# Optimization experiments

Measured on AMD Instinct MI355X. Metric: run time of the kernel, lower is better.

## Reference

```python
import jax, jax.numpy as jnp
import numpy as np

L, N, H_IN, H = 512, 32, 1024, 1024


def _mk_params(key, in_dim, hid):
    ks = jax.random.split(key, 7)
    s_in = 1.0 / np.sqrt(in_dim)
    s_h = 1.0 / np.sqrt(hid)
    return dict(
        Wmx=jax.random.uniform(ks[0], (hid, in_dim), jnp.float32, -s_in, s_in),
        Wmh=jax.random.uniform(ks[1], (hid, hid), jnp.float32, -s_h, s_h),
        bmx=jax.random.uniform(ks[2], (hid,), jnp.float32, -s_in, s_in),
        bmh=jax.random.uniform(ks[3], (hid,), jnp.float32, -s_h, s_h),
        Wgx=jax.random.uniform(ks[4], (4 * hid, in_dim), jnp.float32, -s_in, s_in),
        Wgm=jax.random.uniform(ks[5], (4 * hid, hid), jnp.float32, -s_h, s_h),
        bg=jax.random.uniform(ks[6], (4 * hid,), jnp.float32, -s_h, s_h),
    )


def setup_inputs() -> dict:
    key = jax.random.key(0)
    k_in, k0, k1 = jax.random.split(key, 3)
    inp = {"inputs": jax.random.normal(k_in, (L, N, H_IN), jnp.float32)}
    for i, (k, d) in enumerate([(k0, H_IN), (k1, H)]):
        p = _mk_params(k, d, H)
        for name, v in p.items():
            inp[f"{name}{i}"] = v
    return inp


def _run_layer(xs, state, Wmx, Wmh, bmx, bmh, Wgx, Wgm, bg):
    # xs: (L, N, in_dim); state: ((N,H),(N,H))
    def step(carry, x_t):
        h, c = carry
        m = (x_t @ Wmx.T + bmx) * (h @ Wmh.T + bmh)  # multiplicative intermediate
        g = x_t @ Wgx.T + m @ Wgm.T + bg             # (N, 4H)
        i_g, f_g, z_g, o_g = jnp.split(g, 4, axis=-1)
        c_new = jax.nn.sigmoid(f_g) * c + jax.nn.sigmoid(i_g) * jnp.tanh(z_g)
        h_new = jax.nn.sigmoid(o_g) * jnp.tanh(c_new)
        return (h_new, c_new), h_new

    (h, c), ys = jax.lax.scan(step, state, xs)
    return ys, (h, c)


def reference(inputs, Wmx0, Wmh0, bmx0, bmh0, Wgx0, Wgm0, bg0,
              Wmx1, Wmh1, bmx1, bmh1, Wgx1, Wgm1, bg1):
    zeros = jnp.zeros((N, H), inputs.dtype)
    state = (zeros, zeros)
    # NOTE: original torch code carries hidden_state across layers (quirk kept).
    ys, state = _run_layer(inputs, state, Wmx0, Wmh0, bmx0, bmh0, Wgx0, Wgm0, bg0)
    hs, cs = [state[0]], [state[1]]
    ys, state = _run_layer(ys, state, Wmx1, Wmh1, bmx1, bmh1, Wgx1, Wgm1, bg1)
    hs.append(state[0]); cs.append(state[1])
    return ys, (jnp.stack(hs), jnp.stack(cs))
```

## Files before the change

### kernel.cpp

```cpp
#include <hip/hip_runtime.h>
#include <hip/hip_bf16.h>


typedef unsigned short u16;
typedef unsigned int u32;
typedef unsigned long long u64;
typedef __attribute__((ext_vector_type(8))) short bf16x8;
typedef __attribute__((ext_vector_type(4))) float f32x4;

#define LSEQ 512
#define NB   32
#define HD   1024
#define G4   4096
#define YSZ  (LSEQ*NB*HD)
#define NH32 (NB*HD)
#define SEG  64
#define NSEG (LSEQ/SEG)
#define PERSIST_LDS 163840

#define ATOMIC_RLX __ATOMIC_RELAXED
#define SCOPE_AGT __HIP_MEMORY_SCOPE_AGENT

__device__ __forceinline__ float b2f(u16 u) {
    u32 i = ((u32)u) << 16; float f; __builtin_memcpy(&f, &i, 4); return f;
}
__device__ __forceinline__ u16 f2b(float f) {
    u32 x; __builtin_memcpy(&x, &f, 4);
    return (u16)((x + 0x7fffu + ((x >> 16) & 1u)) >> 16);
}
__device__ __forceinline__ int SW(int row, int byte) { return byte ^ ((row & 7) << 4); }

__device__ __forceinline__ void waitpair(const u32* flags, u32 target) {
    const int lane = threadIdx.x & 63;
    const u64* p = (const u64*)flags + (size_t)lane * 16;
    for (;;) {
        u64 v = __hip_atomic_load(p, ATOMIC_RLX, SCOPE_AGT);
        u32 lo = (u32)v, hi = (u32)(v >> 32);
        if (__all(lo >= target && hi >= target)) break;
    }
    asm volatile("" ::: "memory");
}
__device__ __forceinline__ void signal_slot(u32* flags, int b, int rt, u32 val) {
    asm volatile("s_waitcnt vmcnt(0)" ::: "memory");
    if ((threadIdx.x & 63) == 0)
        __hip_atomic_store(flags + b * 32 + rt, val, ATOMIC_RLX, SCOPE_AGT);
}

__global__ void k_cvt(const float* __restrict__ s, u16* __restrict__ d, long n) {
    long i = (long)blockIdx.x * blockDim.x + threadIdx.x;
    long stride = (long)gridDim.x * blockDim.x;
    for (; i < n; i += stride) d[i] = f2b(s[i]);
}

template<typename XT> __device__ __forceinline__ bf16x8 ld8(const XT* p);
template<> __device__ __forceinline__ bf16x8 ld8<u16>(const u16* p) {
    return *(const bf16x8*)p;
}
template<> __device__ __forceinline__ bf16x8 ld8<float>(const float* p) {
    float4 a = *(const float4*)p, b = *(const float4*)(p + 4);
    bf16x8 r;
    r[0]=(short)f2b(a.x); r[1]=(short)f2b(a.y); r[2]=(short)f2b(a.z); r[3]=(short)f2b(a.w);
    r[4]=(short)f2b(b.x); r[5]=(short)f2b(b.y); r[6]=(short)f2b(b.z); r[7]=(short)f2b(b.w);
    return r;
}

template<typename XT>
__global__ __launch_bounds__(256) void k_gemm(
    const XT* __restrict__ X, const u16* __restrict__ W,
    const float* __restrict__ bias, u16* __restrict__ Out, int ldo)
{
    __shared__ u16 As[128][40];
    __shared__ u16 Bs[128][40];
    int bm = blockIdx.y, bn = blockIdx.x;
    int tid = threadIdx.x;
    int w = tid >> 6, lane = tid & 63;
    int wm = w >> 1, wn = w & 1;
    int l16 = lane & 15, lk = lane >> 4;

    f32x4 acc[4][4];
    #pragma unroll
    for (int i = 0; i < 4; ++i)
        #pragma unroll
        for (int j = 0; j < 4; ++j) acc[i][j] = (f32x4){0.f, 0.f, 0.f, 0.f};

    for (int kt = 0; kt < 32; ++kt) {
        __syncthreads();
        #pragma unroll
        for (int c = 0; c < 2; ++c) {
            int cid = tid + c * 256;
            int rrow = cid >> 2, kc = (cid & 3) * 8;
            *(bf16x8*)(&As[rrow][kc]) = ld8<XT>(X + (long)(bm * 128 + rrow) * HD + kt * 32 + kc);
            *(bf16x8*)(&Bs[rrow][kc]) = ld8<u16>(W + (long)(bn * 128 + rrow) * HD + kt * 32 + kc);
        }
        __syncthreads();
        bf16x8 af[4], bfr[4];
        #pragma unroll
        for (int mt = 0; mt < 4; ++mt)
            af[mt] = *(const bf16x8*)(&As[wm * 64 + mt * 16 + l16][lk * 8]);
        #pragma unroll
        for (int nt = 0; nt < 4; ++nt)
            bfr[nt] = *(const bf16x8*)(&Bs[wn * 64 + nt * 16 + l16][lk * 8]);
        #pragma unroll
        for (int mt = 0; mt < 4; ++mt)
            #pragma unroll
            for (int nt = 0; nt < 4; ++nt)
                acc[mt][nt] = __builtin_amdgcn_mfma_f32_16x16x32_bf16(
                    af[mt], bfr[nt], acc[mt][nt], 0, 0, 0);
    }
    #pragma unroll
    for (int mt = 0; mt < 4; ++mt)
        #pragma unroll
        for (int nt = 0; nt < 4; ++nt) {
            int colg = bn * 128 + wn * 64 + nt * 16 + l16;
            float bv = bias[colg];
            #pragma unroll
            for (int r = 0; r < 4; ++r) {
                int rowg = bm * 128 + wm * 64 + mt * 16 + lk * 4 + r;
                Out[(long)rowg * ldo + colg] = f2b(acc[mt][nt][r] + bv);
            }
        }
}

__global__ __launch_bounds__(256, 1) void k_persist(
    const u16* __restrict__ Wmhb, const float* __restrict__ bmh,
    const u16* __restrict__ Wgmb,
    const u16* __restrict__ Ab,
    const u16* __restrict__ Gxb,
    u16* eh, u16* em,
    float* __restrict__ cbuf,
    u16* __restrict__ yb, float* __restrict__ yf,
    float* __restrict__ tail,
    int l, int tbc, int tbi, u32* fM, u32* fH)
{
    extern __shared__ __align__(16) char lds[];
    const int tid = threadIdx.x;
    const int b = blockIdx.x;
    const int w = tid >> 6, lane = tid & 63;
    const int l16 = lane & 15, lk = lane >> 4;

    for (int it = 0; it < 32; ++it) {
        int cch = tid + it * 256;
        int lr = cch >> 7, k8 = cch & 127;
        int g = lr >> 4, c16 = lr & 15;
        bf16x8 v = *(const bf16x8*)(Wgmb + (long)(g * 1024 + 16 * b + c16) * HD + k8 * 8);
        *(bf16x8*)(lds + SW(lr, lr * 2048 + k8 * 16)) = v;
    }
    for (int it = 0; it < 8; ++it) {
        int cch = tid + it * 256;
        int lr = cch >> 7, k8 = cch & 127;
        bf16x8 v = *(const bf16x8*)(Wmhb + (long)(16 * b + lr) * HD + k8 * 8);
        *(bf16x8*)(lds + 131072 + SW(lr, lr * 2048 + k8 * 16)) = v;
    }
    __syncthreads();

    const int colg = 16 * b + l16;

    if (w >= 2) {
        const int rt = w - 2;
        const float bcol = bmh[colg];
        const u64* hrow = (const u64*)eh + (rt * 16 + l16) * (HD / 4);
        u16* mdst = em + (rt * 16 + lk * 4) * HD + colg;

        for (int t = 0; t < SEG; ++t) {
            const u32 gt = (u32)(tbc + t);
            const u16* At = Ab + (long)(tbi + t) * NH32;
            u16 atv[4];
            #pragma unroll
            for (int r = 0; r < 4; ++r)
                atv[r] = At[(rt * 16 + lk * 4 + r) * HD + colg];
            waitpair(fH, gt);
            u64 hq[64];
            #pragma unroll
            for (int kt = 0; kt < 32; ++kt) {
                hq[2*kt]   = __hip_atomic_load(hrow + kt * 8 + lk * 2,     ATOMIC_RLX, SCOPE_AGT);
                hq[2*kt+1] = __hip_atomic_load(hrow + kt * 8 + lk * 2 + 1, ATOMIC_RLX, SCOPE_AGT);
            }
            __builtin_amdgcn_sched_barrier(0);
            f32x4 acc = (f32x4){0.f, 0.f, 0.f, 0.f};
            #pragma unroll
            for (int kt = 0; kt < 32; ++kt) {
                union { bf16x8 v; u64 q[2]; } u;
                u.q[0] = hq[2*kt]; u.q[1] = hq[2*kt+1];
                bf16x8 bfrag = *(const bf16x8*)(lds + 131072 +
                                SW(l16, l16 * 2048 + kt * 64 + lk * 16));
                acc = __builtin_amdgcn_mfma_f32_16x16x32_bf16(u.v, bfrag, acc, 0, 0, 0);
            }
            #pragma unroll
            for (int r = 0; r < 4; ++r)
                __hip_atomic_store(mdst + r * HD,
                    f2b(b2f(atv[r]) * (acc[r] + bcol)), ATOMIC_RLX, SCOPE_AGT);
            signal_slot(fM, b, rt, gt + 1);
        }
    } else {
        const int rt = w;
        f32x4 creg;
        #pragma unroll
        for (int r = 0; r < 4; ++r)
            creg[r] = cbuf[(rt * 16 + lk * 4 + r) * HD + colg];
        const u64* mrow = (const u64*)em + (rt * 16 + l16) * (HD / 4);

        for (int t = 0; t < SEG; ++t) {
            const u32 gt = (u32)(tbc + t);
            const u16* Gx = Gxb + (long)t * NB * G4;
            u16 gxv[4][4];
            #pragma unroll
            for (int g = 0; g < 4; ++g)
                #pragma unroll
                for (int r = 0; r < 4; ++r)
                    gxv[g][r] = Gx[(long)(rt * 16 + lk * 4 + r) * G4 + g * 1024 + colg];
            waitpair(fM, gt + 1);
            u64 mq[64];
            #pragma unroll
            for (int kt = 0; kt < 32; ++kt) {
                mq[2*kt]   = __hip_atomic_load(mrow + kt * 8 + lk * 2,     ATOMIC_RLX, SCOPE_AGT);
                mq[2*kt+1] = __hip_atomic_load(mrow + kt * 8 + lk * 2 + 1, ATOMIC_RLX, SCOPE_AGT);
            }
            __builtin_amdgcn_sched_barrier(0);
            f32x4 acc[4];
            #pragma unroll
            for (int g = 0; g < 4; ++g) acc[g] = (f32x4){0.f, 0.f, 0.f, 0.f};
            #pragma unroll
            for (int kt = 0; kt < 32; ++kt) {
                union { bf16x8 v; u64 q[2]; } u;
                u.q[0] = mq[2*kt]; u.q[1] = mq[2*kt+1];
                #pragma unroll
                for (int g = 0; g < 4; ++g) {
                    int lr = g * 16 + l16;
                    bf16x8 bfrag = *(const bf16x8*)(lds + SW(lr, lr * 2048 + kt * 64 + lk * 16));
                    acc[g] = __builtin_amdgcn_mfma_f32_16x16x32_bf16(u.v, bfrag, acc[g], 0, 0, 0);
                }
            }
            float hn[4];
            #pragma unroll
            for (int r = 0; r < 4; ++r) {
                int row = rt * 16 + lk * 4 + r;
                float ig = acc[0][r] + b2f(gxv[0][r]);
                float fg = acc[1][r] + b2f(gxv[1][r]);
                float zg = acc[2][r] + b2f(gxv[2][r]);
                float og = acc[3][r] + b2f(gxv[3][r]);
                float si = 1.f / (1.f + expf(-ig));
                float sf = 1.f / (1.f + expf(-fg));
                float so = 1.f / (1.f + expf(-og));
                float cn = sf * creg[r] + si * tanhf(zg);
                hn[r] = so * tanhf(cn);
                creg[r] = cn;
                __hip_atomic_store(eh + (long)row * HD + colg, f2b(hn[r]), ATOMIC_RLX, SCOPE_AGT);
            }
            signal_slot(fH, b, rt, gt + 1);
            #pragma unroll
            for (int r = 0; r < 4; ++r) {
                int row = rt * 16 + lk * 4 + r;
                long yidx = (long)(tbi + t) * NH32 + (long)row * HD + colg;
                if (yb) yb[yidx] = f2b(hn[r]); else yf[yidx] = hn[r];
                if (tbi + t == LSEQ - 1) {
                    tail[(long)l * NH32 + row * HD + colg] = hn[r];
                    tail[2L * NH32 + (long)l * NH32 + row * HD + colg] = creg[r];
                }
            }
        }
        #pragma unroll
        for (int r = 0; r < 4; ++r)
            cbuf[(rt * 16 + lk * 4 + r) * HD + colg] = creg[r];
    }
}

extern "C" void kernel_launch(void* const* d_in, const int* in_sizes, int n_in,
                              void* d_out, int out_size, void* d_ws, size_t ws_size,
                              hipStream_t stream) {
    (void)in_sizes; (void)n_in; (void)out_size; (void)ws_size;
    const float* inputs = (const float*)d_in[0];
    const float* Wmx[2] = {(const float*)d_in[1], (const float*)d_in[8]};
    const float* Wmh[2] = {(const float*)d_in[2], (const float*)d_in[9]};
    const float* bmx[2] = {(const float*)d_in[3], (const float*)d_in[10]};
    const float* bmh[2] = {(const float*)d_in[4], (const float*)d_in[11]};
    const float* Wgx[2] = {(const float*)d_in[5], (const float*)d_in[12]};
    const float* Wgm[2] = {(const float*)d_in[6], (const float*)d_in[13]};
    const float* bg[2]  = {(const float*)d_in[7], (const float*)d_in[14]};
    float* out = (float*)d_out;

    char* ws = (char*)d_ws;
    const long MB = 1024L * 1024L;
    u16* Wmxb[2] = {(u16*)(ws + 0 * MB),  (u16*)(ws + 2 * MB)};
    u16* Wmhb[2] = {(u16*)(ws + 4 * MB),  (u16*)(ws + 6 * MB)};
    u16* Wgxb[2] = {(u16*)(ws + 8 * MB),  (u16*)(ws + 16 * MB)};
    u16* Wgmb[2] = {(u16*)(ws + 24 * MB), (u16*)(ws + 32 * MB)};
    u16* Yb  = (u16*)(ws + 40 * MB);
    u16* Ab  = (u16*)(ws + 72 * MB);
    u16* Gxb = (u16*)(ws + 104 * MB);
    char* ex = ws + 120 * MB;
    u16* exch_h = (u16*)ex;
    u16* exch_m = (u16*)(ex + 65536);
    float* cbuf = (float*)(ex + 131072);
    u32* fM     = (u32*)(ex + 262144);
    u32* fH     = (u32*)(ex + 262144 + 8192);

    hipFuncSetAttribute((const void*)k_persist,
                        hipFuncAttributeMaxDynamicSharedMemorySize, PERSIST_LDS);

    hipMemsetAsync(ex, 0, 262144 + 16384, stream);

    k_cvt<<<512, 256, 0, stream>>>(Wmx[0], Wmxb[0], (long)HD * HD);
    k_cvt<<<512, 256, 0, stream>>>(Wmx[1], Wmxb[1], (long)HD * HD);
    k_cvt<<<512, 256, 0, stream>>>(Wmh[0], Wmhb[0], (long)HD * HD);
    k_cvt<<<512, 256, 0, stream>>>(Wmh[1], Wmhb[1], (long)HD * HD);
    k_cvt<<<1024, 256, 0, stream>>>(Wgx[0], Wgxb[0], (long)G4 * HD);
    k_cvt<<<1024, 256, 0, stream>>>(Wgx[1], Wgxb[1], (long)G4 * HD);
    k_cvt<<<1024, 256, 0, stream>>>(Wgm[0], Wgmb[0], (long)G4 * HD);
    k_cvt<<<1024, 256, 0, stream>>>(Wgm[1], Wgmb[1], (long)G4 * HD);

    for (int l = 0; l < 2; ++l) {
        if (l == 0)
            k_gemm<float><<<dim3(8, 128), 256, 0, stream>>>(inputs, Wmxb[0], bmx[0], Ab, HD);
        else
            k_gemm<u16><<<dim3(8, 128), 256, 0, stream>>>(Yb, Wmxb[1], bmx[1], Ab, HD);
        for (int s = 0; s < NSEG; ++s) {
            if (l == 0)
                k_gemm<float><<<dim3(32, 16), 256, 0, stream>>>(
                    inputs + (long)s * SEG * NB * HD, Wgxb[0], bg[0], Gxb, G4);
            else
                k_gemm<u16><<<dim3(32, 16), 256, 0, stream>>>(
                    Yb + (long)s * SEG * NB * HD, Wgxb[1], bg[1], Gxb, G4);
            k_persist<<<64, 256, PERSIST_LDS, stream>>>(
                Wmhb[l], bmh[l], Wgmb[l], Ab, Gxb,
                exch_h, exch_m, cbuf,
                l ? nullptr : Yb, l ? out : nullptr, out + YSZ,
                l, l * LSEQ + s * SEG, s * SEG, fM, fH);
        }
    }
}
```

Measured before the change: 15.43 ms.

## Split batch into 8-row sub-blocks so each wave runs both m and gate stages

Instead of dedicating two waves to the m = Ax*(Wmh h) stage and two to the gate stage, each wave now handles both stages on different 8-row sub-blocks (sbA for m, sbB for gates), with per-sub-block flags. This aims to pipeline the two dependent stages across sub-blocks so waves no longer sit idle waiting on the other role. It uses 16-row MFMAs with only half the lanes active on output, which wastes MFMA throughput and adds per-step flag polling.

```diff
diff --git a/kernel.cpp b/kernel.cpp
--- a/kernel.cpp
+++ b/kernel.cpp
@@ -30,20 +30,18 @@
 }
 __device__ __forceinline__ int SW(int row, int byte) { return byte ^ ((row & 7) << 4); }
 
-__device__ __forceinline__ void waitpair(const u32* flags, u32 target) {
-    const int lane = threadIdx.x & 63;
-    const u64* p = (const u64*)flags + (size_t)lane * 16;
+__device__ __forceinline__ void poll_sb(const u32* flags, int sb, u32 target) {
+    const u32* p = flags + (threadIdx.x & 63) * 32 + sb;
     for (;;) {
-        u64 v = __hip_atomic_load(p, ATOMIC_RLX, SCOPE_AGT);
-        u32 lo = (u32)v, hi = (u32)(v >> 32);
-        if (__all(lo >= target && hi >= target)) break;
+        u32 v = __hip_atomic_load(p, ATOMIC_RLX, SCOPE_AGT);
+        if (__all(v >= target)) break;
     }
     asm volatile("" ::: "memory");
 }
-__device__ __forceinline__ void signal_slot(u32* flags, int b, int rt, u32 val) {
+__device__ __forceinline__ void sig_sb(u32* flags, int b, int sb, u32 val) {
     asm volatile("s_waitcnt vmcnt(0)" ::: "memory");
     if ((threadIdx.x & 63) == 0)
-        __hip_atomic_store(flags + b * 32 + rt, val, ATOMIC_RLX, SCOPE_AGT);
+        __hip_atomic_store(flags + b * 32 + sb, val, ATOMIC_RLX, SCOPE_AGT);
 }
 
 __global__ void k_cvt(const float* __restrict__ s, u16* __restrict__ d, long n) {
@@ -154,90 +152,91 @@
     __syncthreads();
 
     const int colg = 16 * b + l16;
-
-    if (w >= 2) {
-        const int rt = w - 2;
-        const float bcol = bmh[colg];
-        const u64* hrow = (const u64*)eh + (rt * 16 + l16) * (HD / 4);
-        u16* mdst = em + (rt * 16 + lk * 4) * HD + colg;
-
-        for (int t = 0; t < SEG; ++t) {
-            const u32 gt = (u32)(tbc + t);
-            const u16* At = Ab + (long)(tbi + t) * NH32;
-            u16 atv[4];
+    const int sbA = w;
+    const int sbB = (w + 2) & 3;
+    const float bcol = bmh[colg];
+    const bool act = (lk < 2);
+    const int lr8 = lk * 4;
+
+    f32x4 creg = (f32x4){0.f, 0.f, 0.f, 0.f};
+    if (act)
+        #pragma unroll
+        for (int r = 0; r < 4; ++r)
+            creg[r] = cbuf[(sbB * 8 + lr8 + r) * HD + colg];
+
+    const u64* hrowA = (const u64*)eh + (sbA * 8 + (l16 & 7)) * (HD / 4);
+    const u64* mrowB = (const u64*)em + (sbB * 8 + (l16 & 7)) * (HD / 4);
+
+    for (int t = 0; t < SEG; ++t) {
+        const u32 gt = (u32)(tbc + t);
+        const u16* At = Ab + (long)(tbi + t) * NH32;
+        const u16* Gx = Gxb + (long)t * NB * G4;
+        u16 atv[4];
+        u16 gxv[4][4];
+        #pragma unroll
+        for (int r = 0; r < 4; ++r)
+            atv[r] = At[(sbA * 8 + ((lr8 + r) & 7)) * HD + colg];
+        #pragma unroll
+        for (int g = 0; g < 4; ++g)
             #pragma unroll
             for (int r = 0; r < 4; ++r)
-                atv[r] = At[(rt * 16 + lk * 4 + r) * HD + colg];
-            waitpair(fH, gt);
-            u64 hq[64];
-            #pragma unroll
-            for (int kt = 0; kt < 32; ++kt) {
-                hq[2*kt]   = __hip_atomic_load(hrow + kt * 8 + lk * 2,     ATOMIC_RLX, SCOPE_AGT);
-                hq[2*kt+1] = __hip_atomic_load(hrow + kt * 8 + lk * 2 + 1, ATOMIC_RLX, SCOPE_AGT);
+                gxv[g][r] = Gx[(long)(sbB * 8 + ((lr8 + r) & 7)) * G4 + g * 1024 + colg];
+
+        poll_sb(fH, sbA, gt);
+        u64 hq[64];
+        #pragma unroll
+        for (int kt = 0; kt < 32; ++kt) {
+            hq[2*kt]   = __hip_atomic_load(hrowA + kt * 8 + lk * 2,     ATOMIC_RLX, SCOPE_AGT);
+            hq[2*kt+1] = __hip_atomic_load(hrowA + kt * 8 + lk * 2 + 1, ATOMIC_RLX, SCOPE_AGT);
+        }
+        __builtin_amdgcn_sched_barrier(0);
+        f32x4 acc = (f32x4){0.f, 0.f, 0.f, 0.f};
+        #pragma unroll
+        for (int kt = 0; kt < 32; ++kt) {
+            union { bf16x8 v; u64 q[2]; } u;
+            u.q[0] = hq[2*kt]; u.q[1] = hq[2*kt+1];
+            bf16x8 bfrag = *(const bf16x8*)(lds + 131072 +
+                            SW(l16, l16 * 2048 + kt * 64 + lk * 16));
+            acc = __builtin_amdgcn_mfma_f32_16x16x32_bf16(u.v, bfrag, acc, 0, 0, 0);
+        }
+        if (act)
+            #pragma unroll
+            for (int r = 0; r < 4; ++r)
+                __hip_atomic_store(em + (long)(sbA * 8 + lr8 + r) * HD + colg,
+                    f2b(b2f(atv[r]) * (acc[r] + bcol)), ATOMIC_RLX, SCOPE_AGT);
+        sig_sb(fM, b, sbA, gt + 1);
+
+        poll_sb(fM, sbB, gt + 1);
+        u64 mq[64];
+        #pragma unroll
+        for (int kt = 0; kt < 32; ++kt) {
+            mq[2*kt]   = __hip_atomic_load(mrowB + kt * 8 + lk * 2,     ATOMIC_RLX, SCOPE_AGT);
+            mq[2*kt+1] = __hip_atomic_load(mrowB + kt * 8 + lk * 2 + 1, ATOMIC_RLX, SCOPE_AGT);
+        }
+        __builtin_amdgcn_sched_barrier(0);
+        f32x4 gacc[4];
+        #pragma unroll
+        for (int g = 0; g < 4; ++g) gacc[g] = (f32x4){0.f, 0.f, 0.f, 0.f};
+        #pragma unroll
+        for (int kt = 0; kt < 32; ++kt) {
+            union { bf16x8 v; u64 q[2]; } u;
+            u.q[0] = mq[2*kt]; u.q[1] = mq[2*kt+1];
+            #pragma unroll
+            for (int g = 0; g < 4; ++g) {
+                int lr = g * 16 + l16;
+                bf16x8 bfrag = *(const bf16x8*)(lds + SW(lr, lr * 2048 + kt * 64 + lk * 16));
+                gacc[g] = __builtin_amdgcn_mfma_f32_16x16x32_bf16(u.v, bfrag, gacc[g], 0, 0, 0);
             }
-            __builtin_amdgcn_sched_barrier(0);
-            f32x4 acc = (f32x4){0.f, 0.f, 0.f, 0.f};
-            #pragma unroll
-            for (int kt = 0; kt < 32; ++kt) {
-                union { bf16x8 v; u64 q[2]; } u;
-                u.q[0] = hq[2*kt]; u.q[1] = hq[2*kt+1];
-                bf16x8 bfrag = *(const bf16x8*)(lds + 131072 +
-                                SW(l16, l16 * 2048 + kt * 64 + lk * 16));
-                acc = __builtin_amdgcn_mfma_f32_16x16x32_bf16(u.v, bfrag, acc, 0, 0, 0);
-            }
-            #pragma unroll
-            for (int r = 0; r < 4; ++r)
-                __hip_atomic_store(mdst + r * HD,
-                    f2b(b2f(atv[r]) * (acc[r] + bcol)), ATOMIC_RLX, SCOPE_AGT);
-            signal_slot(fM, b, rt, gt + 1);
-        }
-    } else {
-        const int rt = w;
-        f32x4 creg;
-        #pragma unroll
-        for (int r = 0; r < 4; ++r)
-            creg[r] = cbuf[(rt * 16 + lk * 4 + r) * HD + colg];
-        const u64* mrow = (const u64*)em + (rt * 16 + l16) * (HD / 4);
-
-        for (int t = 0; t < SEG; ++t) {
-            const u32 gt = (u32)(tbc + t);
-            const u16* Gx = Gxb + (long)t * NB * G4;
-            u16 gxv[4][4];
-            #pragma unroll
-            for (int g = 0; g < 4; ++g)
-                #pragma unroll
-                for (int r = 0; r < 4; ++r)
-                    gxv[g][r] = Gx[(long)(rt * 16 + lk * 4 + r) * G4 + g * 1024 + colg];
-            waitpair(fM, gt + 1);
-            u64 mq[64];
-            #pragma unroll
-            for (int kt = 0; kt < 32; ++kt) {
-                mq[2*kt]   = __hip_atomic_load(mrow + kt * 8 + lk * 2,     ATOMIC_RLX, SCOPE_AGT);
-                mq[2*kt+1] = __hip_atomic_load(mrow + kt * 8 + lk * 2 + 1, ATOMIC_RLX, SCOPE_AGT);
-            }
-            __builtin_amdgcn_sched_barrier(0);
-            f32x4 acc[4];
-            #pragma unroll
-            for (int g = 0; g < 4; ++g) acc[g] = (f32x4){0.f, 0.f, 0.f, 0.f};
-            #pragma unroll
-            for (int kt = 0; kt < 32; ++kt) {
-                union { bf16x8 v; u64 q[2]; } u;
-                u.q[0] = mq[2*kt]; u.q[1] = mq[2*kt+1];
-                #pragma unroll
-                for (int g = 0; g < 4; ++g) {
-                    int lr = g * 16 + l16;
-                    bf16x8 bfrag = *(const bf16x8*)(lds + SW(lr, lr * 2048 + kt * 64 + lk * 16));
-                    acc[g] = __builtin_amdgcn_mfma_f32_16x16x32_bf16(u.v, bfrag, acc[g], 0, 0, 0);
-                }
-            }
-            float hn[4];
+        }
+        float hn[4];
+        if (act) {
             #pragma unroll
             for (int r = 0; r < 4; ++r) {
-                int row = rt * 16 + lk * 4 + r;
-                float ig = acc[0][r] + b2f(gxv[0][r]);
-                float fg = acc[1][r] + b2f(gxv[1][r]);
-                float zg = acc[2][r] + b2f(gxv[2][r]);
-                float og = acc[3][r] + b2f(gxv[3][r]);
+                int row = sbB * 8 + lr8 + r;
+                float ig = gacc[0][r] + b2f(gxv[0][r]);
+                float fg = gacc[1][r] + b2f(gxv[1][r]);
+                float zg = gacc[2][r] + b2f(gxv[2][r]);
+                float og = gacc[3][r] + b2f(gxv[3][r]);
                 float si = 1.f / (1.f + expf(-ig));
                 float sf = 1.f / (1.f + expf(-fg));
                 float so = 1.f / (1.f + expf(-og));
@@ -246,10 +245,12 @@
                 creg[r] = cn;
                 __hip_atomic_store(eh + (long)row * HD + colg, f2b(hn[r]), ATOMIC_RLX, SCOPE_AGT);
             }
-            signal_slot(fH, b, rt, gt + 1);
+        }
+        sig_sb(fH, b, sbB, gt + 1);
+        if (act) {
             #pragma unroll
             for (int r = 0; r < 4; ++r) {
-                int row = rt * 16 + lk * 4 + r;
+                int row = sbB * 8 + lr8 + r;
                 long yidx = (long)(tbi + t) * NH32 + (long)row * HD + colg;
                 if (yb) yb[yidx] = f2b(hn[r]); else yf[yidx] = hn[r];
                 if (tbi + t == LSEQ - 1) {
@@ -258,10 +259,11 @@
                 }
             }
         }
+    }
+    if (act)
         #pragma unroll
         for (int r = 0; r < 4; ++r)
-            cbuf[(rt * 16 + lk * 4 + r) * HD + colg] = creg[r];
-    }
+            cbuf[(sbB * 8 + lr8 + r) * HD + colg] = creg[r];
 }
 
 extern "C" void kernel_launch(void* const* d_in, const int* in_sizes, int n_in,
```

Result: slower. 20.22 ms (+31.1%).

## Poll flags with one wave per block and broadcast via block barriers

Applied to the files above, without the earlier changes.

Before, every wave polled the global flag array itself. Now only one wave per block polls (with s_sleep backoff) and then releases the other waves through __syncthreads. The two role-specialised loops are merged into one loop, so all waves go through the same barriers each step. This cuts global polling traffic, but it adds two block-wide barriers per timestep and removes overlap between the m-producing and gate-computing waves inside a block.

```diff
diff --git a/kernel.cpp b/kernel.cpp
--- a/kernel.cpp
+++ b/kernel.cpp
@@ -30,20 +30,16 @@
 }
 __device__ __forceinline__ int SW(int row, int byte) { return byte ^ ((row & 7) << 4); }
 
-__device__ __forceinline__ void waitpair(const u32* flags, u32 target) {
+__device__ __forceinline__ void pollwait(const u32* flags, u32 target) {
     const int lane = threadIdx.x & 63;
     const u64* p = (const u64*)flags + (size_t)lane * 16;
     for (;;) {
         u64 v = __hip_atomic_load(p, ATOMIC_RLX, SCOPE_AGT);
         u32 lo = (u32)v, hi = (u32)(v >> 32);
         if (__all(lo >= target && hi >= target)) break;
+        __builtin_amdgcn_s_sleep(4);
     }
     asm volatile("" ::: "memory");
-}
-__device__ __forceinline__ void signal_slot(u32* flags, int b, int rt, u32 val) {
-    asm volatile("s_waitcnt vmcnt(0)" ::: "memory");
-    if ((threadIdx.x & 63) == 0)
-        __hip_atomic_store(flags + b * 32 + rt, val, ATOMIC_RLX, SCOPE_AGT);
 }
 
 __global__ void k_cvt(const float* __restrict__ s, u16* __restrict__ d, long n) {
@@ -154,21 +150,39 @@
     __syncthreads();
 
     const int colg = 16 * b + l16;
-
-    if (w >= 2) {
-        const int rt = w - 2;
-        const float bcol = bmh[colg];
-        const u64* hrow = (const u64*)eh + (rt * 16 + l16) * (HD / 4);
-        u16* mdst = em + (rt * 16 + lk * 4) * HD + colg;
-
-        for (int t = 0; t < SEG; ++t) {
-            const u32 gt = (u32)(tbc + t);
+    const int rt = w & 1;
+    const bool isP1 = (w >= 2);
+
+    const float bcol = bmh[colg];
+    const u64* hrow = (const u64*)eh + (rt * 16 + l16) * (HD / 4);
+    u16* mdst = em + (rt * 16 + lk * 4) * HD + colg;
+    const u64* mrow = (const u64*)em + (rt * 16 + l16) * (HD / 4);
+    f32x4 creg = (f32x4){0.f, 0.f, 0.f, 0.f};
+    if (!isP1)
+        #pragma unroll
+        for (int r = 0; r < 4; ++r)
+            creg[r] = cbuf[(rt * 16 + lk * 4 + r) * HD + colg];
+
+    for (int t = 0; t < SEG; ++t) {
+        const u32 gt = (u32)(tbc + t);
+        u16 atv[4];
+        u16 gxv[4][4];
+        if (isP1) {
             const u16* At = Ab + (long)(tbi + t) * NH32;
-            u16 atv[4];
             #pragma unroll
             for (int r = 0; r < 4; ++r)
                 atv[r] = At[(rt * 16 + lk * 4 + r) * HD + colg];
-            waitpair(fH, gt);
+        } else {
+            const u16* Gx = Gxb + (long)t * NB * G4;
+            #pragma unroll
+            for (int g = 0; g < 4; ++g)
+                #pragma unroll
+                for (int r = 0; r < 4; ++r)
+                    gxv[g][r] = Gx[(long)(rt * 16 + lk * 4 + r) * G4 + g * 1024 + colg];
+        }
+        if (w == 2) pollwait(fH, gt);
+        __syncthreads();
+        if (isP1) {
             u64 hq[64];
             #pragma unroll
             for (int kt = 0; kt < 32; ++kt) {
@@ -189,26 +203,13 @@
             for (int r = 0; r < 4; ++r)
                 __hip_atomic_store(mdst + r * HD,
                     f2b(b2f(atv[r]) * (acc[r] + bcol)), ATOMIC_RLX, SCOPE_AGT);
-            signal_slot(fM, b, rt, gt + 1);
-        }
-    } else {
-        const int rt = w;
-        f32x4 creg;
-        #pragma unroll
-        for (int r = 0; r < 4; ++r)
-            creg[r] = cbuf[(rt * 16 + lk * 4 + r) * HD + colg];
-        const u64* mrow = (const u64*)em + (rt * 16 + l16) * (HD / 4);
-
-        for (int t = 0; t < SEG; ++t) {
-            const u32 gt = (u32)(tbc + t);
-            const u16* Gx = Gxb + (long)t * NB * G4;
-            u16 gxv[4][4];
-            #pragma unroll
-            for (int g = 0; g < 4; ++g)
-                #pragma unroll
-                for (int r = 0; r < 4; ++r)
-                    gxv[g][r] = Gx[(long)(rt * 16 + lk * 4 + r) * G4 + g * 1024 + colg];
-            waitpair(fM, gt + 1);
+            asm volatile("s_waitcnt vmcnt(0)" ::: "memory");
+            if (lane == 0)
+                __hip_atomic_store(fM + b * 32 + rt, gt + 1, ATOMIC_RLX, SCOPE_AGT);
+        }
+        if (w == 0) pollwait(fM, gt + 1);
+        __syncthreads();
+        if (!isP1) {
             u64 mq[64];
             #pragma unroll
             for (int kt = 0; kt < 32; ++kt) {
@@ -216,9 +217,9 @@
                 mq[2*kt+1] = __hip_atomic_load(mrow + kt * 8 + lk * 2 + 1, ATOMIC_RLX, SCOPE_AGT);
             }
             __builtin_amdgcn_sched_barrier(0);
-            f32x4 acc[4];
-            #pragma unroll
-            for (int g = 0; g < 4; ++g) acc[g] = (f32x4){0.f, 0.f, 0.f, 0.f};
+            f32x4 gacc[4];
+            #pragma unroll
+            for (int g = 0; g < 4; ++g) gacc[g] = (f32x4){0.f, 0.f, 0.f, 0.f};
             #pragma unroll
             for (int kt = 0; kt < 32; ++kt) {
                 union { bf16x8 v; u64 q[2]; } u;
@@ -227,17 +228,17 @@
                 for (int g = 0; g < 4; ++g) {
                     int lr = g * 16 + l16;
                     bf16x8 bfrag = *(const bf16x8*)(lds + SW(lr, lr * 2048 + kt * 64 + lk * 16));
-                    acc[g] = __builtin_amdgcn_mfma_f32_16x16x32_bf16(u.v, bfrag, acc[g], 0, 0, 0);
+                    gacc[g] = __builtin_amdgcn_mfma_f32_16x16x32_bf16(u.v, bfrag, gacc[g], 0, 0, 0);
                 }
             }
             float hn[4];
             #pragma unroll
             for (int r = 0; r < 4; ++r) {
                 int row = rt * 16 + lk * 4 + r;
-                float ig = acc[0][r] + b2f(gxv[0][r]);
-                float fg = acc[1][r] + b2f(gxv[1][r]);
-                float zg = acc[2][r] + b2f(gxv[2][r]);
-                float og = acc[3][r] + b2f(gxv[3][r]);
+                float ig = gacc[0][r] + b2f(gxv[0][r]);
+                float fg = gacc[1][r] + b2f(gxv[1][r]);
+                float zg = gacc[2][r] + b2f(gxv[2][r]);
+                float og = gacc[3][r] + b2f(gxv[3][r]);
                 float si = 1.f / (1.f + expf(-ig));
                 float sf = 1.f / (1.f + expf(-fg));
                 float so = 1.f / (1.f + expf(-og));
@@ -246,7 +247,9 @@
                 creg[r] = cn;
                 __hip_atomic_store(eh + (long)row * HD + colg, f2b(hn[r]), ATOMIC_RLX, SCOPE_AGT);
             }
-            signal_slot(fH, b, rt, gt + 1);
+            asm volatile("s_waitcnt vmcnt(0)" ::: "memory");
+            if (lane == 0)
+                __hip_atomic_store(fH + b * 32 + rt, gt + 1, ATOMIC_RLX, SCOPE_AGT);
             #pragma unroll
             for (int r = 0; r < 4; ++r) {
                 int row = rt * 16 + lk * 4 + r;
@@ -258,10 +261,11 @@
                 }
             }
         }
+    }
+    if (!isP1)
         #pragma unroll
         for (int r = 0; r < 4; ++r)
             cbuf[(rt * 16 + lk * 4 + r) * HD + colg] = creg[r];
-    }
 }
 
 extern "C" void kernel_launch(void* const* d_in, const int* in_sizes, int n_in,
```

After: 15.41 ms. Within noise of the previous version (-0.1%).

## Replace flag-based sync with parity bits embedded in exchanged bf16 data

Applied to the files above, without the earlier changes.

Drops the separate per-block flag arrays and their wait/signal steps. Each step's parity is written into the low mantissa bit of every exchanged bf16 value for h and m, and consumers spin-load the data until every word carries the expected parity. This removes the store fence and the flag round trip on every recurrent step, so producer-to-consumer latency on the critical path should shrink. In exchange it loses one mantissa bit of precision and relies on 8-byte atomic loads observing the 16-bit stores consistently.

```diff
diff --git a/kernel.cpp b/kernel.cpp
--- a/kernel.cpp
+++ b/kernel.cpp
@@ -20,6 +20,7 @@
 
 #define ATOMIC_RLX __ATOMIC_RELAXED
 #define SCOPE_AGT __HIP_MEMORY_SCOPE_AGENT
+#define PAR_MASK 0x0001000100010001ULL
 
 __device__ __forceinline__ float b2f(u16 u) {
     u32 i = ((u32)u) << 16; float f; __builtin_memcpy(&f, &i, 4); return f;
@@ -30,22 +31,10 @@
 }
 __device__ __forceinline__ int SW(int row, int byte) { return byte ^ ((row & 7) << 4); }
 
-__device__ __forceinline__ void waitpair(const u32* flags, u32 target) {
-    const int lane = threadIdx.x & 63;
-    const u64* p = (const u64*)flags + (size_t)lane * 16;
-    for (;;) {
-        u64 v = __hip_atomic_load(p, ATOMIC_RLX, SCOPE_AGT);
-        u32 lo = (u32)v, hi = (u32)(v >> 32);
-        if (__all(lo >= target && hi >= target)) break;
-    }
-    asm volatile("" ::: "memory");
-}
-__device__ __forceinline__ void signal_slot(u32* flags, int b, int rt, u32 val) {
-    asm volatile("s_waitcnt vmcnt(0)" ::: "memory");
-    if ((threadIdx.x & 63) == 0)
-        __hip_atomic_store(flags + b * 32 + rt, val, ATOMIC_RLX, SCOPE_AGT);
-}
-
+__global__ void k_fill(u32* __restrict__ d, int n, u32 v) {
+    int i = blockIdx.x * blockDim.x + threadIdx.x;
+    if (i < n) d[i] = v;
+}
 __global__ void k_cvt(const float* __restrict__ s, u16* __restrict__ d, long n) {
     long i = (long)blockIdx.x * blockDim.x + threadIdx.x;
     long stride = (long)gridDim.x * blockDim.x;
@@ -130,7 +119,7 @@
     float* __restrict__ cbuf,
     u16* __restrict__ yb, float* __restrict__ yf,
     float* __restrict__ tail,
-    int l, int tbc, int tbi, u32* fM, u32* fH)
+    int l, int tbc, int tbi)
 {
     extern __shared__ __align__(16) char lds[];
     const int tid = threadIdx.x;
@@ -163,17 +152,25 @@
 
         for (int t = 0; t < SEG; ++t) {
             const u32 gt = (u32)(tbc + t);
+            const u64 exph = ((gt & 1u) == 0) ? PAR_MASK : 0ULL;
+            const u16 pm = (u16)(gt & 1u);
             const u16* At = Ab + (long)(tbi + t) * NH32;
             u16 atv[4];
             #pragma unroll
             for (int r = 0; r < 4; ++r)
                 atv[r] = At[(rt * 16 + lk * 4 + r) * HD + colg];
-            waitpair(fH, gt);
             u64 hq[64];
-            #pragma unroll
-            for (int kt = 0; kt < 32; ++kt) {
-                hq[2*kt]   = __hip_atomic_load(hrow + kt * 8 + lk * 2,     ATOMIC_RLX, SCOPE_AGT);
-                hq[2*kt+1] = __hip_atomic_load(hrow + kt * 8 + lk * 2 + 1, ATOMIC_RLX, SCOPE_AGT);
+            for (;;) {
+                #pragma unroll
+                for (int kt = 0; kt < 32; ++kt) {
+                    hq[2*kt]   = __hip_atomic_load(hrow + kt * 8 + lk * 2,     ATOMIC_RLX, SCOPE_AGT);
+                    hq[2*kt+1] = __hip_atomic_load(hrow + kt * 8 + lk * 2 + 1, ATOMIC_RLX, SCOPE_AGT);
+                }
+                u64 d = 0;
+                #pragma unroll
+                for (int j = 0; j < 64; ++j) d |= (hq[j] ^ exph);
+                if (__all((d & PAR_MASK) == 0)) break;
+                __builtin_amdgcn_s_sleep(1);
             }
             __builtin_amdgcn_sched_barrier(0);
             f32x4 acc = (f32x4){0.f, 0.f, 0.f, 0.f};
@@ -186,10 +183,10 @@
                 acc = __builtin_amdgcn_mfma_f32_16x16x32_bf16(u.v, bfrag, acc, 0, 0, 0);
             }
             #pragma unroll
-            for (int r = 0; r < 4; ++r)
-                __hip_atomic_store(mdst + r * HD,
-                    f2b(b2f(atv[r]) * (acc[r] + bcol)), ATOMIC_RLX, SCOPE_AGT);
-            signal_slot(fM, b, rt, gt + 1);
+            for (int r = 0; r < 4; ++r) {
+                u16 v = (u16)((f2b(b2f(atv[r]) * (acc[r] + bcol)) & 0xFFFEu) | pm);
+                __hip_atomic_store(mdst + r * HD, v, ATOMIC_RLX, SCOPE_AGT);
+            }
         }
     } else {
         const int rt = w;
@@ -201,6 +198,8 @@
 
         for (int t = 0; t < SEG; ++t) {
             const u32 gt = (u32)(tbc + t);
+            const u64 expm = (gt & 1u) ? PAR_MASK : 0ULL;
+            const u16 pm = (u16)(gt & 1u);
             const u16* Gx = Gxb + (long)t * NB * G4;
             u16 gxv[4][4];
             #pragma unroll
@@ -208,17 +207,23 @@
                 #pragma unroll
                 for (int r = 0; r < 4; ++r)
                     gxv[g][r] = Gx[(long)(rt * 16 + lk * 4 + r) * G4 + g * 1024 + colg];
-            waitpair(fM, gt + 1);
             u64 mq[64];
-            #pragma unroll
-            for (int kt = 0; kt < 32; ++kt) {
-                mq[2*kt]   = __hip_atomic_load(mrow + kt * 8 + lk * 2,     ATOMIC_RLX, SCOPE_AGT);
-                mq[2*kt+1] = __hip_atomic_load(mrow + kt * 8 + lk * 2 + 1, ATOMIC_RLX, SCOPE_AGT);
+            for (;;) {
+                #pragma unroll
+                for (int kt = 0; kt < 32; ++kt) {
+                    mq[2*kt]   = __hip_atomic_load(mrow + kt * 8 + lk * 2,     ATOMIC_RLX, SCOPE_AGT);
+                    mq[2*kt+1] = __hip_atomic_load(mrow + kt * 8 + lk * 2 + 1, ATOMIC_RLX, SCOPE_AGT);
+                }
+                u64 d = 0;
+                #pragma unroll
+                for (int j = 0; j < 64; ++j) d |= (mq[j] ^ expm);
+                if (__all((d & PAR_MASK) == 0)) break;
+                __builtin_amdgcn_s_sleep(1);
             }
             __builtin_amdgcn_sched_barrier(0);
-            f32x4 acc[4];
-            #pragma unroll
-            for (int g = 0; g < 4; ++g) acc[g] = (f32x4){0.f, 0.f, 0.f, 0.f};
+            f32x4 gacc[4];
+            #pragma unroll
+            for (int g = 0; g < 4; ++g) gacc[g] = (f32x4){0.f, 0.f, 0.f, 0.f};
             #pragma unroll
             for (int kt = 0; kt < 32; ++kt) {
                 union { bf16x8 v; u64 q[2]; } u;
@@ -227,26 +232,26 @@
                 for (int g = 0; g < 4; ++g) {
                     int lr = g * 16 + l16;
                     bf16x8 bfrag = *(const bf16x8*)(lds + SW(lr, lr * 2048 + kt * 64 + lk * 16));
-                    acc[g] = __builtin_amdgcn_mfma_f32_16x16x32_bf16(u.v, bfrag, acc[g], 0, 0, 0);
+                    gacc[g] = __builtin_amdgcn_mfma_f32_16x16x32_bf16(u.v, bfrag, gacc[g], 0, 0, 0);
                 }
             }
             float hn[4];
             #pragma unroll
             for (int r = 0; r < 4; ++r) {
                 int row = rt * 16 + lk * 4 + r;
-                float ig = acc[0][r] + b2f(gxv[0][r]);
-                float fg = acc[1][r] + b2f(gxv[1][r]);
-                float zg = acc[2][r] + b2f(gxv[2][r]);
-                float og = acc[3][r] + b2f(gxv[3][r]);
+                float ig = gacc[0][r] + b2f(gxv[0][r]);
+                float fg = gacc[1][r] + b2f(gxv[1][r]);
+                float zg = gacc[2][r] + b2f(gxv[2][r]);
+                float og = gacc[3][r] + b2f(gxv[3][r]);
                 float si = 1.f / (1.f + expf(-ig));
                 float sf = 1.f / (1.f + expf(-fg));
                 float so = 1.f / (1.f + expf(-og));
                 float cn = sf * creg[r] + si * tanhf(zg);
                 hn[r] = so * tanhf(cn);
                 creg[r] = cn;
-                __hip_atomic_store(eh + (long)row * HD + colg, f2b(hn[r]), ATOMIC_RLX, SCOPE_AGT);
-            }
-            signal_slot(fH, b, rt, gt + 1);
+                u16 v = (u16)((f2b(hn[r]) & 0xFFFEu) | pm);
+                __hip_atomic_store(eh + (long)row * HD + colg, v, ATOMIC_RLX, SCOPE_AGT);
+            }
             #pragma unroll
             for (int r = 0; r < 4; ++r) {
                 int row = rt * 16 + lk * 4 + r;
@@ -291,13 +296,12 @@
     u16* exch_h = (u16*)ex;
     u16* exch_m = (u16*)(ex + 65536);
     float* cbuf = (float*)(ex + 131072);
-    u32* fM     = (u32*)(ex + 262144);
-    u32* fH     = (u32*)(ex + 262144 + 8192);
 
     hipFuncSetAttribute((const void*)k_persist,
                         hipFuncAttributeMaxDynamicSharedMemorySize, PERSIST_LDS);
 
-    hipMemsetAsync(ex, 0, 262144 + 16384, stream);
+    k_fill<<<128, 256, 0, stream>>>((u32*)ex, 32768, 0x00010001u);
+    hipMemsetAsync(cbuf, 0, 131072, stream);
 
     k_cvt<<<512, 256, 0, stream>>>(Wmx[0], Wmxb[0], (long)HD * HD);
     k_cvt<<<512, 256, 0, stream>>>(Wmx[1], Wmxb[1], (long)HD * HD);
@@ -324,7 +328,7 @@
                 Wmhb[l], bmh[l], Wgmb[l], Ab, Gxb,
                 exch_h, exch_m, cbuf,
                 l ? nullptr : Yb, l ? out : nullptr, out + YSZ,
-                l, l * LSEQ + s * SEG, s * SEG, fM, fH);
-        }
-    }
-}
+                l, l * LSEQ + s * SEG, s * SEG);
+        }
+    }
+}
```

Measured after the change: 31.81 ms. +106.2%, slower.
